# Optimization experiments

Hardware: AMD Instinct MI355X
Metric: run time of the kernel (lower is better)

Reference implementation:

```python
import jax, jax.numpy as jnp
import numpy as np

HIDDEN = 32
FF = 40

def _glorot(key, shape):
    fan_in, fan_out = shape[0], shape[1]
    lim = np.sqrt(6.0 / (fan_in + fan_out)).astype(np.float32)
    return jax.random.uniform(key, shape, jnp.float32, -lim, lim)

def setup_inputs() -> dict:
    key = jax.random.key(0)
    ks = jax.random.split(key, 9)
    B, T = 16384, 512
    inputs = jax.random.normal(ks[0], (B, T, 1), dtype=jnp.float32)
    return {
        "inputs": inputs,
        "W1hh": _glorot(ks[1], (1 + HIDDEN, FF)),
        "b1hh": jnp.zeros((FF,), jnp.float32),
        "W2hh": _glorot(ks[2], (FF, HIDDEN)),
        "b2hh": jnp.zeros((HIDDEN,), jnp.float32),
        "W1ho": _glorot(ks[3], (1 + HIDDEN, FF)),
        "b1ho": jnp.zeros((FF,), jnp.float32),
        "W2ho": _glorot(ks[4], (FF, 1)),
        "b2ho": jnp.zeros((1,), jnp.float32),
    }

def reference(inputs, W1hh, b1hh, W2hh, b2hh, W1ho, b1ho, W2ho, b2ho):
    B = inputs.shape[0]
    h0 = jnp.zeros((B, HIDDEN), inputs.dtype)
    xs = jnp.transpose(inputs, (1, 0, 2))  # [T, B, 1]

    def step(h, u):
        c = jnp.concatenate([h, u], axis=1)            # [B, 33]
        out = jax.nn.sigmoid(c @ W1ho + b1ho) @ W2ho + b2ho  # [B, 1]
        h_new = jax.nn.sigmoid(c @ W1hh + b1hh) @ W2hh + b2hh  # [B, 32]
        return h_new, out[:, 0]

    _, ys = jax.lax.scan(step, h0, xs)  # ys: [T, B]
    return ys.T  # [B, T]
```

## Files before the change

### kernel.cpp

```cpp
#include <hip/hip_runtime.h>

#define HIDDEN 32
#define FF 40
#define SEQ_T 512
#define RD 16

typedef _Float16 half8 __attribute__((ext_vector_type(8)));
typedef __attribute__((ext_vector_type(4))) float float4v;
typedef __attribute__((ext_vector_type(4))) unsigned uint4v;
typedef __attribute__((ext_vector_type(2))) unsigned uint2v;


__global__ __launch_bounds__(256, 1) void rnn_prep(
    const float* __restrict__ W1hh, const float* __restrict__ b1hh,
    const float* __restrict__ W2hh, const float* __restrict__ b2hh,
    const float* __restrict__ W1ho, const float* __restrict__ b1ho,
    unsigned short* __restrict__ acatP)
{
    const int idx = blockIdx.x * 256 + threadIdx.x;
    if (idx >= 96 * 64) return;
    const int mrow = idx >> 6, s = idx & 63;

    const bool hh = mrow < 48;
    const int col = hh ? mrow : mrow - 48;
    float val = 0.f;
    if (col < FF && s < 42) {
        const float* W1 = hh ? W1hh : W1ho;
        const float* b1 = hh ? b1hh : b1ho;
        if (s < FF) {
            for (int i = 0; i < HIDDEN; ++i)
                val = __builtin_fmaf(W2hh[s * HIDDEN + i], W1[i * FF + col], val);
        } else if (s == 40) {
            val = W1[HIDDEN * FF + col];
        } else {
            val = b1[col];
            for (int i = 0; i < HIDDEN; ++i)
                val = __builtin_fmaf(b2hh[i], W1[i * FF + col], val);
        }
    }
    const _Float16 hv = (_Float16)val;
    acatP[idx] = __builtin_bit_cast(unsigned short, hv);
}

__device__ __forceinline__ float sigmoid_fast(float x) {
    const float e = __builtin_amdgcn_exp2f(-x * 1.44269504088896341f);
    return __builtin_amdgcn_rcpf(1.0f + e);
}

__device__ __forceinline__ unsigned cvt_pkrtz_u(float a, float b) {
    auto h = __builtin_amdgcn_cvt_pkrtz(a, b);
    return __builtin_bit_cast(unsigned, h);
}

__global__ __launch_bounds__(256, 2) void rnn_main(
    const float* __restrict__ inputs,
    const unsigned short* __restrict__ acatP,
    const float* __restrict__ W1hh, const float* __restrict__ b1hh,
    const float* __restrict__ W1ho, const float* __restrict__ b1ho,
    const float* __restrict__ W2ho, const float* __restrict__ b2ho,
    float* __restrict__ ys)
{
    __shared__ __align__(16) unsigned short ring[RD][32][72];

    const int tid = threadIdx.x;
    const int wv  = __builtin_amdgcn_readfirstlane(tid >> 6);
    const bool producer = (wv < 2);
    const int hi  = wv & 1;
    const int l = tid & 63;
    const int r = l & 15;
    const int g = l >> 4;
    const int rr = hi * 16 + r;
    const size_t rowbase = ((size_t)blockIdx.x * 32 + rr) * SEQ_T;
    const float* __restrict__ in_row = inputs + rowbase;

    if (producer) __builtin_amdgcn_s_setprio(1);

    {
        uint4v* zp = (uint4v*)&ring[0][0][0];
        const uint4v z4 = {0u, 0u, 0u, 0u};
#pragma unroll
        for (int i = 0; i < 18; ++i)
            zp[tid + 256 * i] = z4;
    }

    half8 A[3][2];
    const int mb = producer ? 0 : 3;
#pragma unroll
    for (int mt = 0; mt < 3; ++mt)
#pragma unroll
        for (int ks = 0; ks < 2; ++ks)
            A[mt][ks] = *(const half8*)(acatP + ((mb + mt) * 16 + r) * 64 + ks * 32 + g * 8);

    float w2o_l[3][4];
#pragma unroll
    for (int mt = 0; mt < 3; ++mt)
#pragma unroll
        for (int q = 0; q < 4; ++q) {
            const int j = 16 * mt + 4 * g + q;
            w2o_l[mt][q] = (j < FF) ? W2ho[j] : 0.f;
        }
    const float b2o = b2ho[0];
    const bool out16 = (l < 16);

    auto load_frags = [&](int sl, half8 (&f)[2]) {
        const unsigned short* p = &ring[sl][rr][0];
        f[0] = *(const half8*)(p + g * 8);
        f[1] = *(const half8*)(p + 32 + g * 8);
    };

    auto do_mfma = [&](const half8 (&f)[2], float4v (&acc)[3]) {
#pragma unroll
        for (int mt = 0; mt < 3; ++mt) {
            float4v a = (float4v)0.f;
            a = __builtin_amdgcn_mfma_f32_16x16x32_f16(A[mt][0], f[0], a, 0, 0, 0);
            a = __builtin_amdgcn_mfma_f32_16x16x32_f16(A[mt][1], f[1], a, 0, 0, 0);
            acc[mt] = a;
        }
    };

    auto store_s = [&](int slot, const float4v (&z)[3], float u_next) {
        unsigned* bp = (unsigned*)&ring[slot][rr][0];
#pragma unroll
        for (int mt = 0; mt < 3; ++mt) {
            const float s0 = sigmoid_fast(z[mt][0]);
            const float s1 = sigmoid_fast(z[mt][1]);
            const float s2 = sigmoid_fast(z[mt][2]);
            const float s3 = sigmoid_fast(z[mt][3]);
            const unsigned p01 = cvt_pkrtz_u(s0, s1);
            const unsigned p23 = cvt_pkrtz_u(s2, s3);
            const int j = 4 * mt + g;
            if (j < 10) {
                uint2v hp;
                hp.x = p01; hp.y = p23;
                *(uint2v*)(bp + 2 * j) = hp;
            }
        }
        if (g == 3) bp[20] = cvt_pkrtz_u(u_next, 1.0f);
    };

    __syncthreads();

    float uc[6];
    if (producer) {
        const float u0 = in_row[0];
        float4v z[3];
#pragma unroll
        for (int mt = 0; mt < 3; ++mt)
#pragma unroll
            for (int q = 0; q < 4; ++q) {
                const int n = 16 * mt + 4 * g + q;
                const int nc = n < FF ? n : FF - 1;
                z[mt][q] = __builtin_fmaf(u0, W1hh[HIDDEN * FF + nc], b1hh[nc]);
            }
        store_s(0, z, in_row[1]);
#pragma unroll
        for (int i = 0; i < 6; ++i) uc[i] = in_row[2 + i];
    } else {
        const float u0 = in_row[0];
        float op = 0.f;
#pragma unroll
        for (int mt = 0; mt < 3; ++mt)
#pragma unroll
            for (int q = 0; q < 4; ++q) {
                const int n = 16 * mt + 4 * g + q;
                const int nc = n < FF ? n : FF - 1;
                const float so = sigmoid_fast(
                    __builtin_fmaf(u0, W1ho[HIDDEN * FF + nc], b1ho[nc]));
                op = __builtin_fmaf(so, w2o_l[mt][q], op);
            }
        op += __shfl_xor(op, 16);
        op += __shfl_xor(op, 32);
        if (out16) ys[rowbase] = op + b2o;
    }
    __syncthreads();

    for (int p = 0; p < 87; ++p) {
        if (producer) {
            const int tb = 6 * p + 1;
            float un[6];
#pragma unroll
            for (int i = 0; i < 6; ++i) {
                int tn = tb + 7 + i;
                tn = tn < SEQ_T ? tn : SEQ_T - 1;
                un[i] = in_row[tn];
            }
#pragma unroll
            for (int i = 0; i < 6; ++i) {
                const int t = tb + i;
                if (t < SEQ_T) {
                    half8 f[2];
                    load_frags((t - 1) & (RD - 1), f);
                    float4v z[3];
                    do_mfma(f, z);
                    store_s(t & (RD - 1), z, uc[i]);
                }
            }
#pragma unroll
            for (int i = 0; i < 6; ++i) uc[i] = un[i];
        } else {
#pragma unroll
            for (int i = 0; i < 6; ++i) {
                const int t = 6 * p - 5 + i;
                if (t >= 1 && t < SEQ_T) {
                    half8 f[2];
                    load_frags((t - 1) & (RD - 1), f);
                    float4v acc[3];
                    do_mfma(f, acc);
                    float op = 0.f;
#pragma unroll
                    for (int mt = 0; mt < 3; ++mt)
#pragma unroll
                        for (int q = 0; q < 4; ++q)
                            op = __builtin_fmaf(sigmoid_fast(acc[mt][q]),
                                                w2o_l[mt][q], op);
                    op += __shfl_xor(op, 16);
                    op += __shfl_xor(op, 32);
                    if (out16) ys[rowbase + t] = op + b2o;
                }
            }
        }
        __syncthreads();
    }
}

extern "C" void kernel_launch(void* const* d_in, const int* in_sizes, int n_in,
                              void* d_out, int out_size, void* d_ws, size_t ws_size,
                              hipStream_t stream) {
    const float* inputs = (const float*)d_in[0];
    const float* W1hh   = (const float*)d_in[1];
    const float* b1hh   = (const float*)d_in[2];
    const float* W2hh   = (const float*)d_in[3];
    const float* b2hh   = (const float*)d_in[4];
    const float* W1ho   = (const float*)d_in[5];
    const float* b1ho   = (const float*)d_in[6];
    const float* W2ho   = (const float*)d_in[7];
    const float* b2ho   = (const float*)d_in[8];
    float* ys = (float*)d_out;

    unsigned short* acatP = (unsigned short*)d_ws;

    const int B = in_sizes[0] / SEQ_T;

    rnn_prep<<<(96 * 64 + 255) / 256, 256, 0, stream>>>(
        W1hh, b1hh, W2hh, b2hh, W1ho, b1ho, acatP);

    const int blocks = B / 32;
    rnn_main<<<blocks, 256, 0, stream>>>(
        inputs, acatP, W1hh, b1hh, W1ho, b1ho, W2ho, b2ho, ys);
}
```

Baseline: 334.6 us.

## Fold weight-precompute prep kernel into main kernel via shared memory

Removes the separate rnn_prep launch. Each block of the main kernel now stages the raw weights in the shared ring buffer, computes the fused fp16 A-matrix itself, and loads its MFMA fragments from there. The aim is to drop one kernel launch and the dependency between the two kernels. The cost is that all 512 blocks repeat the roughly 6K-element precompute, which adds startup latency to each block.

```diff
diff --git a/kernel.cpp b/kernel.cpp
--- a/kernel.cpp
+++ b/kernel.cpp
@@ -11,37 +11,6 @@
 typedef __attribute__((ext_vector_type(2))) unsigned uint2v;
 
 
-__global__ __launch_bounds__(256, 1) void rnn_prep(
-    const float* __restrict__ W1hh, const float* __restrict__ b1hh,
-    const float* __restrict__ W2hh, const float* __restrict__ b2hh,
-    const float* __restrict__ W1ho, const float* __restrict__ b1ho,
-    unsigned short* __restrict__ acatP)
-{
-    const int idx = blockIdx.x * 256 + threadIdx.x;
-    if (idx >= 96 * 64) return;
-    const int mrow = idx >> 6, s = idx & 63;
-
-    const bool hh = mrow < 48;
-    const int col = hh ? mrow : mrow - 48;
-    float val = 0.f;
-    if (col < FF && s < 42) {
-        const float* W1 = hh ? W1hh : W1ho;
-        const float* b1 = hh ? b1hh : b1ho;
-        if (s < FF) {
-            for (int i = 0; i < HIDDEN; ++i)
-                val = __builtin_fmaf(W2hh[s * HIDDEN + i], W1[i * FF + col], val);
-        } else if (s == 40) {
-            val = W1[HIDDEN * FF + col];
-        } else {
-            val = b1[col];
-            for (int i = 0; i < HIDDEN; ++i)
-                val = __builtin_fmaf(b2hh[i], W1[i * FF + col], val);
-        }
-    }
-    const _Float16 hv = (_Float16)val;
-    acatP[idx] = __builtin_bit_cast(unsigned short, hv);
-}
-
 __device__ __forceinline__ float sigmoid_fast(float x) {
     const float e = __builtin_amdgcn_exp2f(-x * 1.44269504088896341f);
     return __builtin_amdgcn_rcpf(1.0f + e);
@@ -52,10 +21,18 @@
     return __builtin_bit_cast(unsigned, h);
 }
 
+#define W2HH_OFF 0
+#define W1HH_OFF 1280
+#define B1HH_OFF 2600
+#define W1HO_OFF 2640
+#define B1HO_OFF 3960
+#define B2HH_OFF 4000
+#define ACATP_BYTE_OFF 32768
+
 __global__ __launch_bounds__(256, 2) void rnn_main(
     const float* __restrict__ inputs,
-    const unsigned short* __restrict__ acatP,
     const float* __restrict__ W1hh, const float* __restrict__ b1hh,
+    const float* __restrict__ W2hh, const float* __restrict__ b2hh,
     const float* __restrict__ W1ho, const float* __restrict__ b1ho,
     const float* __restrict__ W2ho, const float* __restrict__ b2ho,
     float* __restrict__ ys)
@@ -75,6 +52,59 @@
 
     if (producer) __builtin_amdgcn_s_setprio(1);
 
+    float* wl = (float*)&ring[0][0][0];
+    unsigned short* ap = (unsigned short*)((char*)&ring[0][0][0] + ACATP_BYTE_OFF);
+
+    for (int i = tid; i < 1280; i += 256) wl[W2HH_OFF + i] = W2hh[i];
+    for (int i = tid; i < 1320; i += 256) wl[W1HH_OFF + i] = W1hh[i];
+    for (int i = tid; i < 1320; i += 256) wl[W1HO_OFF + i] = W1ho[i];
+    if (tid < 40) wl[B1HH_OFF + tid] = b1hh[tid];
+    if (tid < 40) wl[B1HO_OFF + tid] = b1ho[tid];
+    if (tid < 32) wl[B2HH_OFF + tid] = b2hh[tid];
+    __syncthreads();
+
+    {
+        const int s = tid & 63;
+        float w2row[HIDDEN];
+        if (s < FF)
+#pragma unroll
+            for (int i = 0; i < HIDDEN; ++i) w2row[i] = wl[W2HH_OFF + s * HIDDEN + i];
+#pragma unroll 4
+        for (int j = 0; j < 24; ++j) {
+            const int idx = tid + 256 * j;
+            const int mrow = idx >> 6;
+            const bool hh = mrow < 48;
+            const int col = hh ? mrow : mrow - 48;
+            float val = 0.f;
+            if (col < FF && s < 42) {
+                const float* W1 = wl + (hh ? W1HH_OFF : W1HO_OFF);
+                const float* b1 = wl + (hh ? B1HH_OFF : B1HO_OFF);
+                if (s < FF) {
+                    for (int i = 0; i < HIDDEN; ++i)
+                        val = __builtin_fmaf(w2row[i], W1[i * FF + col], val);
+                } else if (s == 40) {
+                    val = W1[HIDDEN * FF + col];
+                } else {
+                    val = b1[col];
+                    for (int i = 0; i < HIDDEN; ++i)
+                        val = __builtin_fmaf(wl[B2HH_OFF + i], W1[i * FF + col], val);
+                }
+            }
+            const _Float16 hv = (_Float16)val;
+            ap[idx] = __builtin_bit_cast(unsigned short, hv);
+        }
+    }
+    __syncthreads();
+
+    half8 A[3][2];
+    const int mb = producer ? 0 : 3;
+#pragma unroll
+    for (int mt = 0; mt < 3; ++mt)
+#pragma unroll
+        for (int ks = 0; ks < 2; ++ks)
+            A[mt][ks] = *(const half8*)(ap + ((mb + mt) * 16 + r) * 64 + ks * 32 + g * 8);
+    __syncthreads();
+
     {
         uint4v* zp = (uint4v*)&ring[0][0][0];
         const uint4v z4 = {0u, 0u, 0u, 0u};
@@ -82,14 +112,6 @@
         for (int i = 0; i < 18; ++i)
             zp[tid + 256 * i] = z4;
     }
-
-    half8 A[3][2];
-    const int mb = producer ? 0 : 3;
-#pragma unroll
-    for (int mt = 0; mt < 3; ++mt)
-#pragma unroll
-        for (int ks = 0; ks < 2; ++ks)
-            A[mt][ks] = *(const half8*)(acatP + ((mb + mt) * 16 + r) * 64 + ks * 32 + g * 8);
 
     float w2o_l[3][4];
 #pragma unroll
@@ -237,14 +259,9 @@
     const float* b2ho   = (const float*)d_in[8];
     float* ys = (float*)d_out;
 
-    unsigned short* acatP = (unsigned short*)d_ws;
-
     const int B = in_sizes[0] / SEQ_T;
-
-    rnn_prep<<<(96 * 64 + 255) / 256, 256, 0, stream>>>(
-        W1hh, b1hh, W2hh, b2hh, W1ho, b1ho, acatP);
 
     const int blocks = B / 32;
     rnn_main<<<blocks, 256, 0, stream>>>(
-        inputs, acatP, W1hh, b1hh, W1ho, b1ho, W2ho, b2ho, ys);
-}
+        inputs, W1hh, b1hh, W2hh, b2hh, W1ho, b1ho, W2ho, b2ho, ys);
+}
```

Result: slower. 347.3 us (+3.8%).
